# Kernel tuning notes

Hardware: AMD Instinct MI355X
Metric: run time of the kernel (lower is better)

The kernel has to match this reference:

```python
import jax, jax.numpy as jnp
from jax import lax
import numpy as np

LATENT = 16
HIDDEN = 16  # latent_dim > 8 -> 16
NUM_ATTRACTORS = 64
GRAVITY = 0.01
INPUT_DIM = 300
B, S = 32, 2048
N_ITERS = 20


def setup_inputs() -> dict:
    key = jax.random.key(0)
    ks = jax.random.split(key, 12)
    sc = lambda fan_in: 1.0 / np.sqrt(fan_in)
    return {
        "inputs": jax.random.normal(ks[0], (B, S, INPUT_DIM), dtype=jnp.float32),
        "enc_w1": jax.random.normal(ks[1], (INPUT_DIM, HIDDEN), dtype=jnp.float32) * sc(INPUT_DIM),
        "enc_b1": jnp.zeros((HIDDEN,), dtype=jnp.float32),
        "enc_w2": jax.random.normal(ks[2], (HIDDEN, LATENT), dtype=jnp.float32) * sc(HIDDEN),
        "enc_b2": jnp.zeros((LATENT,), dtype=jnp.float32),
        "attractors": jax.random.normal(ks[3], (NUM_ATTRACTORS, LATENT), dtype=jnp.float32) * 0.1,
        "dec_w1": jax.random.normal(ks[4], (LATENT, HIDDEN), dtype=jnp.float32) * sc(LATENT),
        "dec_b1": jnp.zeros((HIDDEN,), dtype=jnp.float32),
        "dec_w2": jax.random.normal(ks[5], (HIDDEN, INPUT_DIM), dtype=jnp.float32) * sc(HIDDEN),
        "dec_b2": jnp.zeros((INPUT_DIM,), dtype=jnp.float32),
        "mass_w": jax.random.normal(ks[6], (LATENT, 1), dtype=jnp.float32) * sc(LATENT),
        "mass_b": jnp.zeros((1,), dtype=jnp.float32),
    }


def reference(inputs, enc_w1, enc_b1, enc_w2, enc_b2, attractors,
              dec_w1, dec_b1, dec_w2, dec_b2, mass_w, mass_b):
    b, s, _ = inputs.shape
    # encoder: Linear(300,16) -> ReLU -> Linear(16,latent)
    h = jax.nn.relu(jnp.einsum('bsi,ih->bsh', inputs, enc_w1) + enc_b1)
    emb = jnp.einsum('bsh,hd->bsd', h, enc_w2) + enc_b2  # [B,S,D]

    def step(pos, _):
        # pos: [B,S,D]; attractors: [A,D]
        diff = attractors[None, None, :, :] - pos[:, :, None, :]          # [B,S,A,D]
        dist = jnp.sqrt(jnp.sum(diff * diff, axis=-1, keepdims=True)) + 1e-6
        forces = jnp.sum(GRAVITY * diff / (dist * dist), axis=2)          # [B,S,D]
        new_pos = pos + 0.1 * forces
        change = jnp.sqrt(jnp.sum((new_pos - pos) ** 2))
        return new_pos, change

    # torch code breaks if change < 1e-6; with random data this never fires,
    # so the fixed 20-iteration scan is equivalent.
    positions, changes = lax.scan(step, emb, None, length=N_ITERS)

    attractor_field = positions.mean(axis=1)                              # [B,D]
    rec = jax.nn.relu(attractor_field @ dec_w1 + dec_b1) @ dec_w2 + dec_b2  # [B,300]
    reconstructions = jnp.broadcast_to(rec[:, None, :], (b, s, INPUT_DIM))
    masses = jax.nn.sigmoid(attractor_field @ mass_w + mass_b)            # [B,1]
    final_change = changes[-1]
    return attractor_field, reconstructions, masses, final_change
```

## Files before the change

### kernel.cpp

```cpp
#include <hip/hip_runtime.h>
#include <cmath>

#define BB 32
#define SS 2048
#define IND 300
#define HID 16
#define LAT 16
#define NA 64
#define NITER 20
#define GRAV 0.01f

#define OFF_FIELD 0
#define OFF_REC   512
#define OFF_MASS  (512 + BB*SS*IND)
#define OFF_CHG   (OFF_MASS + BB)

#define WS_FIELD 0
#define WS_CHG   512

typedef __attribute__((ext_vector_type(8))) __bf16 bf16x8;
typedef __attribute__((ext_vector_type(4))) __bf16 bf16x4;
typedef __attribute__((ext_vector_type(4))) float f32x4;

#define XST 328
#define HST 40
#define WTS 88

__global__ __launch_bounds__(256, 1)
void k_enc_grav(const float* __restrict__ x, const float* __restrict__ w1,
                const float* __restrict__ b1, const float* __restrict__ w2,
                const float* __restrict__ b2, const float* __restrict__ att,
                float* __restrict__ ws)
{
    __shared__ __align__(16) char smem[64 * XST * 2 + 4 * 16 * HST * 2];
    __bf16* xs = (__bf16*)smem;
    __bf16* hl = (__bf16*)(smem + 64 * XST * 2);
    __bf16* Wl = (__bf16*)smem;

    const int tid  = threadIdx.x;
    const int wave = tid >> 6, lane = tid & 63;
    const int quad = lane >> 4, col = lane & 15;
    const int tok0 = blockIdx.x * 64;

    {
        const f32x4* xg = (const f32x4*)(x + (size_t)tok0 * IND);
        #pragma unroll
        for (int i = 0; i < 19; ++i) {
            const int idx = i * 256 + tid;
            if (idx < 4800) {
                f32x4 v = xg[idx];
                const int row = idx / 75, c4 = idx - row * 75;
                bf16x4 b;
                #pragma unroll
                for (int e = 0; e < 4; ++e) b[e] = (__bf16)v[e];
                *(bf16x4*)(xs + row * XST + c4 * 4) = b;
            }
        }
        if (tid < 64) {
            #pragma unroll
            for (int c = 0; c < 20; ++c) xs[tid * XST + 300 + c] = (__bf16)0.f;
        }
    }

    bf16x8 w1f[10];
    #pragma unroll
    for (int s = 0; s < 10; ++s)
        #pragma unroll
        for (int j = 0; j < 8; ++j) {
            const int k = s * 32 + quad * 8 + j;
            w1f[s][j] = (k < IND) ? (__bf16)w1[k * HID + col] : (__bf16)0.f;
        }
    __syncthreads();

    {
        const float b1c = b1[col];
        f32x4 hacc = {b1c, b1c, b1c, b1c};
        const __bf16* myx = xs + (wave * 16 + col) * XST + quad * 8;
        #pragma unroll
        for (int s = 0; s < 10; ++s) {
            bf16x8 af = *(const bf16x8*)(myx + s * 32);
            hacc = __builtin_amdgcn_mfma_f32_16x16x32_bf16(af, w1f[s], hacc, 0, 0, 0);
        }
        __bf16* myh = hl + wave * 16 * HST;
        #pragma unroll
        for (int r = 0; r < 4; ++r)
            myh[(quad * 4 + r) * HST + col] = (__bf16)fmaxf(hacc[r], 0.f);
    }

    f32x4 p;
    {
        bf16x8 w2tf;
        #pragma unroll
        for (int j = 0; j < 8; ++j) {
            const int k = quad * 8 + j;
            w2tf[j] = (k < HID) ? (__bf16)w2[k * LAT + col] : (__bf16)0.f;
        }
        bf16x8 bh;
        #pragma unroll
        for (int e = 0; e < 8; ++e) bh[e] = (__bf16)0.f;
        if (quad < 2)
            bh = *(const bf16x8*)(hl + wave * 16 * HST + col * HST + quad * 8);
        f32x4 pacc = *(const f32x4*)(b2 + quad * 4);
        p = __builtin_amdgcn_mfma_f32_16x16x32_bf16(w2tf, bh, pacc, 0, 0, 0);
    }
    __syncthreads();

    const f32x4 zf = {0.f, 0.f, 0.f, 0.f};
    bf16x8 ones8;
    #pragma unroll
    for (int e = 0; e < 8; ++e) ones8[e] = (__bf16)1.0f;

    bf16x8 aS[4];
    #pragma unroll
    for (int i = 0; i < 4; ++i) {
        f32x4 av = *(const f32x4*)(att + (16 * i + col) * LAT + quad * 4);
        #pragma unroll
        for (int m = 0; m < 4; ++m) {
            aS[i][2 * m]     = (__bf16)(-2.0f * av[m]);
            aS[i][2 * m + 1] = (__bf16)1.0f;
        }
    }
    f32x4 sanv[4];
    {
        float nrm[4];
        #pragma unroll
        for (int i = 0; i < 4; ++i) {
            const float* ar = att + (16 * i + col) * LAT;
            float s = 0.f;
            #pragma unroll
            for (int k = 0; k < LAT; ++k) s = fmaf(ar[k], ar[k], s);
            nrm[i] = s;
        }
        #pragma unroll
        for (int i = 0; i < 4; ++i)
            #pragma unroll
            for (int r = 0; r < 4; ++r)
                sanv[i][r] = __shfl(nrm[i], 16 * quad + quad * 4 + r);
    }
    bf16x8 aF[2];
    #pragma unroll
    for (int h = 0; h < 2; ++h)
        #pragma unroll
        for (int j = 0; j < 8; ++j)
            aF[h][j] = (__bf16)att[(32 * h + quad * 8 + j) * LAT + col];

    __bf16* myW = Wl + wave * 16 * WTS;

    float cd = 0.f;
    #pragma unroll 1
    for (int it = 0; it < NITER; ++it) {
        bf16x8 bp;
        #pragma unroll
        for (int m = 0; m < 4; ++m) {
            float v = p[m];
            bp[2 * m]     = (__bf16)v;
            bp[2 * m + 1] = (__bf16)(v * v);
        }
        f32x4 sf[4];
        #pragma unroll
        for (int i = 0; i < 4; ++i)
            sf[i] = __builtin_amdgcn_mfma_f32_16x16x32_bf16(aS[i], bp, zf, 0, 0, 0);

        #pragma unroll
        for (int i = 0; i < 4; ++i) {
            bf16x4 wp;
            #pragma unroll
            for (int r = 0; r < 4; ++r)
                wp[r] = (__bf16)__builtin_amdgcn_rcpf(sf[i][r] + sanv[i][r]);
            *(bf16x4*)(myW + col * WTS + 16 * i + quad * 4) = wp;
        }
        bf16x8 bw0 = *(bf16x8*)(myW + col * WTS + quad * 8);
        bf16x8 bw1 = *(bf16x8*)(myW + col * WTS + 32 + quad * 8);

        f32x4 F  = __builtin_amdgcn_mfma_f32_16x16x32_bf16(aF[0], bw0, zf, 0, 0, 0);
        F  = __builtin_amdgcn_mfma_f32_16x16x32_bf16(aF[1], bw1, F,  0, 0, 0);
        f32x4 F2 = __builtin_amdgcn_mfma_f32_16x16x32_bf16(ones8, bw0, zf, 0, 0, 0);
        F2 = __builtin_amdgcn_mfma_f32_16x16x32_bf16(ones8, bw1, F2, 0, 0, 0);

        const bool last = (it == NITER - 1);
        #pragma unroll
        for (int r = 0; r < 4; ++r) {
            float np = fmaf(p[r], fmaf(F2[r], -0.1f * GRAV, 1.0f),
                            (0.1f * GRAV) * F[r]);
            if (last) { float d = np - p[r]; cd = fmaf(d, d, cd); }
            p[r] = np;
        }
    }

    f32x4 fs = p;
    #pragma unroll
    for (int m = 1; m <= 8; m <<= 1)
        #pragma unroll
        for (int r = 0; r < 4; ++r) fs[r] += __shfl_xor(fs[r], m);
    const int b = blockIdx.x >> 5;
    if (col == 0) {
        #pragma unroll
        for (int r = 0; r < 4; ++r)
            atomicAdd(ws + WS_FIELD + b * LAT + quad * 4 + r, fs[r]);
    }
    float c2 = cd;
    c2 += __shfl_xor(c2, 1);  c2 += __shfl_xor(c2, 2);  c2 += __shfl_xor(c2, 4);
    c2 += __shfl_xor(c2, 8);  c2 += __shfl_xor(c2, 16); c2 += __shfl_xor(c2, 32);
    if (lane == 0) atomicAdd(ws + WS_CHG, c2);
}

#define CHUNK 8192
#define CPB   (SS * IND / CHUNK)
__global__ __launch_bounds__(256)
void k_bcast(const float* __restrict__ dw1, const float* __restrict__ db1,
             const float* __restrict__ dw2, const float* __restrict__ db2,
             const float* __restrict__ mw,  const float* __restrict__ mb,
             const float* __restrict__ ws, float* __restrict__ out)
{
    __shared__ float sf[LAT];
    __shared__ float sh[HID];
    __shared__ __align__(16) float srow[IND];
    const int blk = blockIdx.x;
    const int b = blk / CPB, c = blk % CPB;
    const int t = threadIdx.x;

    if (t < LAT) {
        float f = ws[WS_FIELD + b * LAT + t] * (1.f / SS);
        sf[t] = f;
        if (c == 0) out[OFF_FIELD + b * LAT + t] = f;
    }
    __syncthreads();
    if (t < HID) {
        float a = db1[t];
        #pragma unroll
        for (int d = 0; d < LAT; ++d) a = fmaf(sf[d], dw1[d * HID + t], a);
        sh[t] = fmaxf(a, 0.f);
    }
    if (c == 0 && t == 32) {
        float a = mb[0];
        #pragma unroll
        for (int d = 0; d < LAT; ++d) a = fmaf(sf[d], mw[d], a);
        out[OFF_MASS + b] = 1.f / (1.f + expf(-a));
    }
    if (blk == 0 && t == 33) out[OFF_CHG] = sqrtf(ws[WS_CHG]);
    __syncthreads();
    if (t < IND) {
        float a = db2[t];
        #pragma unroll
        for (int j = 0; j < HID; ++j) a = fmaf(sh[j], dw2[j * IND + t], a);
        srow[t] = a;
    }
    if (t < IND - 256) {
        const int tc = t + 256;
        float a2 = db2[tc];
        #pragma unroll
        for (int j = 0; j < HID; ++j) a2 = fmaf(sh[j], dw2[j * IND + tc], a2);
        srow[tc] = a2;
    }
    __syncthreads();
    f32x4* o = (f32x4*)(out + OFF_REC + (size_t)b * (SS * IND) + (size_t)c * CHUNK);
    #pragma unroll
    for (int i = 0; i < CHUNK / 4 / 256; ++i) {
        const int o4 = i * 256 + t;
        const int r  = (c * CHUNK + o4 * 4) % IND;
        f32x4 v = *(const f32x4*)(srow + r);
        __builtin_nontemporal_store(v, o + o4);
    }
}

extern "C" void kernel_launch(void* const* d_in, const int* in_sizes, int n_in,
                              void* d_out, int out_size, void* d_ws, size_t ws_size,
                              hipStream_t stream)
{
    const float* x   = (const float*)d_in[0];
    const float* ew1 = (const float*)d_in[1];
    const float* eb1 = (const float*)d_in[2];
    const float* ew2 = (const float*)d_in[3];
    const float* eb2 = (const float*)d_in[4];
    const float* att = (const float*)d_in[5];
    const float* dw1 = (const float*)d_in[6];
    const float* db1 = (const float*)d_in[7];
    const float* dw2 = (const float*)d_in[8];
    const float* db2 = (const float*)d_in[9];
    const float* mw  = (const float*)d_in[10];
    const float* mb  = (const float*)d_in[11];
    float* out = (float*)d_out;
    float* ws  = (float*)d_ws;

    (void)hipMemsetAsync(ws, 0, (WS_CHG + 1) * sizeof(float), stream);
    k_enc_grav<<<BB * SS / 64, 256, 0, stream>>>(x, ew1, eb1, ew2, eb2, att, ws);
    k_bcast<<<BB * CPB, 256, 0, stream>>>(dw1, db1, dw2, db2, mw, mb, ws, out);
}
```

Baseline: 234.0 us.

## Split encoder and gravity loop into separate kernels, two token tiles per wave

The fused encoder+gravity kernel is split in two. The encoder writes latent positions to a scratch area inside the output's reconstruction region. A new gravity kernel then processes two 16-token tiles per wave, interleaving their MFMA chains to hide latency. The encoder kernel no longer carries the iteration loop, and the gravity kernel uses less LDS, so their occupancy can differ. In exchange it adds a global round trip for positions and an extra launch, and it relies on k_bcast overwriting the scratch region afterwards.

Measured after the change: 223.2 us. 1.05x faster.

```diff
diff --git a/kernel.cpp b/kernel.cpp
--- a/kernel.cpp
+++ b/kernel.cpp
@@ -27,15 +27,13 @@
 #define WTS 88
 
 __global__ __launch_bounds__(256, 1)
-void k_enc_grav(const float* __restrict__ x, const float* __restrict__ w1,
-                const float* __restrict__ b1, const float* __restrict__ w2,
-                const float* __restrict__ b2, const float* __restrict__ att,
-                float* __restrict__ ws)
+void k_enc(const float* __restrict__ x, const float* __restrict__ w1,
+           const float* __restrict__ b1, const float* __restrict__ w2,
+           const float* __restrict__ b2, float* __restrict__ pbuf)
 {
     __shared__ __align__(16) char smem[64 * XST * 2 + 4 * 16 * HST * 2];
     __bf16* xs = (__bf16*)smem;
     __bf16* hl = (__bf16*)(smem + 64 * XST * 2);
-    __bf16* Wl = (__bf16*)smem;
 
     const int tid  = threadIdx.x;
     const int wave = tid >> 6, lane = tid & 63;
@@ -103,7 +101,17 @@
         f32x4 pacc = *(const f32x4*)(b2 + quad * 4);
         p = __builtin_amdgcn_mfma_f32_16x16x32_bf16(w2tf, bh, pacc, 0, 0, 0);
     }
-    __syncthreads();
+    ((f32x4*)pbuf)[(size_t)(tok0 + wave * 16 + col) * 4 + quad] = p;
+}
+
+__global__ __launch_bounds__(256, 1)
+void k_grav(const float* __restrict__ att, const float* __restrict__ pbuf,
+            float* __restrict__ ws)
+{
+    __shared__ __bf16 Wl[4][2][16 * WTS];
+    const int tid  = threadIdx.x;
+    const int wave = tid >> 6, lane = tid & 63;
+    const int quad = lane >> 4, col = lane & 15;
 
     const f32x4 zf = {0.f, 0.f, 0.f, 0.f};
     bf16x8 ones8;
@@ -144,55 +152,74 @@
         for (int j = 0; j < 8; ++j)
             aF[h][j] = (__bf16)att[(32 * h + quad * 8 + j) * LAT + col];
 
-    __bf16* myW = Wl + wave * 16 * WTS;
+    const int t0 = blockIdx.x * 128 + wave * 32 + col;
+    f32x4 p[2];
+    p[0] = ((const f32x4*)pbuf)[(size_t)t0 * 4 + quad];
+    p[1] = ((const f32x4*)pbuf)[(size_t)(t0 + 16) * 4 + quad];
+
+    __bf16* myW[2] = { &Wl[wave][0][0], &Wl[wave][1][0] };
 
     float cd = 0.f;
     #pragma unroll 1
     for (int it = 0; it < NITER; ++it) {
-        bf16x8 bp;
-        #pragma unroll
-        for (int m = 0; m < 4; ++m) {
-            float v = p[m];
-            bp[2 * m]     = (__bf16)v;
-            bp[2 * m + 1] = (__bf16)(v * v);
-        }
-        f32x4 sf[4];
-        #pragma unroll
-        for (int i = 0; i < 4; ++i)
-            sf[i] = __builtin_amdgcn_mfma_f32_16x16x32_bf16(aS[i], bp, zf, 0, 0, 0);
-
-        #pragma unroll
-        for (int i = 0; i < 4; ++i) {
-            bf16x4 wp;
-            #pragma unroll
-            for (int r = 0; r < 4; ++r)
-                wp[r] = (__bf16)__builtin_amdgcn_rcpf(sf[i][r] + sanv[i][r]);
-            *(bf16x4*)(myW + col * WTS + 16 * i + quad * 4) = wp;
-        }
-        bf16x8 bw0 = *(bf16x8*)(myW + col * WTS + quad * 8);
-        bf16x8 bw1 = *(bf16x8*)(myW + col * WTS + 32 + quad * 8);
-
-        f32x4 F  = __builtin_amdgcn_mfma_f32_16x16x32_bf16(aF[0], bw0, zf, 0, 0, 0);
-        F  = __builtin_amdgcn_mfma_f32_16x16x32_bf16(aF[1], bw1, F,  0, 0, 0);
-        f32x4 F2 = __builtin_amdgcn_mfma_f32_16x16x32_bf16(ones8, bw0, zf, 0, 0, 0);
-        F2 = __builtin_amdgcn_mfma_f32_16x16x32_bf16(ones8, bw1, F2, 0, 0, 0);
+        bf16x8 bp[2];
+        #pragma unroll
+        for (int s = 0; s < 2; ++s)
+            #pragma unroll
+            for (int m = 0; m < 4; ++m) {
+                float v = p[s][m];
+                bp[s][2 * m]     = (__bf16)v;
+                bp[s][2 * m + 1] = (__bf16)(v * v);
+            }
+        f32x4 sf[2][4];
+        #pragma unroll
+        for (int s = 0; s < 2; ++s)
+            #pragma unroll
+            for (int i = 0; i < 4; ++i)
+                sf[s][i] = __builtin_amdgcn_mfma_f32_16x16x32_bf16(aS[i], bp[s], zf, 0, 0, 0);
+
+        #pragma unroll
+        for (int s = 0; s < 2; ++s)
+            #pragma unroll
+            for (int i = 0; i < 4; ++i) {
+                bf16x4 wp;
+                #pragma unroll
+                for (int r = 0; r < 4; ++r)
+                    wp[r] = (__bf16)__builtin_amdgcn_rcpf(sf[s][i][r] + sanv[i][r]);
+                *(bf16x4*)(myW[s] + col * WTS + 16 * i + quad * 4) = wp;
+            }
+        bf16x8 bw[2][2];
+        #pragma unroll
+        for (int s = 0; s < 2; ++s)
+            #pragma unroll
+            for (int h = 0; h < 2; ++h)
+                bw[s][h] = *(bf16x8*)(myW[s] + col * WTS + 32 * h + quad * 8);
 
         const bool last = (it == NITER - 1);
         #pragma unroll
-        for (int r = 0; r < 4; ++r) {
-            float np = fmaf(p[r], fmaf(F2[r], -0.1f * GRAV, 1.0f),
-                            (0.1f * GRAV) * F[r]);
-            if (last) { float d = np - p[r]; cd = fmaf(d, d, cd); }
-            p[r] = np;
-        }
-    }
-
-    f32x4 fs = p;
+        for (int s = 0; s < 2; ++s) {
+            f32x4 F  = __builtin_amdgcn_mfma_f32_16x16x32_bf16(aF[0], bw[s][0], zf, 0, 0, 0);
+            F  = __builtin_amdgcn_mfma_f32_16x16x32_bf16(aF[1], bw[s][1], F,  0, 0, 0);
+            f32x4 F2 = __builtin_amdgcn_mfma_f32_16x16x32_bf16(ones8, bw[s][0], zf, 0, 0, 0);
+            F2 = __builtin_amdgcn_mfma_f32_16x16x32_bf16(ones8, bw[s][1], F2, 0, 0, 0);
+            #pragma unroll
+            for (int r = 0; r < 4; ++r) {
+                float np = fmaf(p[s][r], fmaf(F2[r], -0.1f * GRAV, 1.0f),
+                                (0.1f * GRAV) * F[r]);
+                if (last) { float d = np - p[s][r]; cd = fmaf(d, d, cd); }
+                p[s][r] = np;
+            }
+        }
+    }
+
+    f32x4 fs;
+    #pragma unroll
+    for (int r = 0; r < 4; ++r) fs[r] = p[0][r] + p[1][r];
     #pragma unroll
     for (int m = 1; m <= 8; m <<= 1)
         #pragma unroll
         for (int r = 0; r < 4; ++r) fs[r] += __shfl_xor(fs[r], m);
-    const int b = blockIdx.x >> 5;
+    const int b = blockIdx.x >> 4;
     if (col == 0) {
         #pragma unroll
         for (int r = 0; r < 4; ++r)
@@ -281,8 +308,10 @@
     const float* mb  = (const float*)d_in[11];
     float* out = (float*)d_out;
     float* ws  = (float*)d_ws;
+    float* pbuf = out + OFF_REC;
 
     (void)hipMemsetAsync(ws, 0, (WS_CHG + 1) * sizeof(float), stream);
-    k_enc_grav<<<BB * SS / 64, 256, 0, stream>>>(x, ew1, eb1, ew2, eb2, att, ws);
+    k_enc <<<BB * SS / 64, 256, 0, stream>>>(x, ew1, eb1, ew2, eb2, pbuf);
+    k_grav<<<BB * SS / 128, 256, 0, stream>>>(att, pbuf, ws);
     k_bcast<<<BB * CPB, 256, 0, stream>>>(dw1, db1, dw2, db2, mw, mb, ws, out);
 }
```
